# Performance work log

Hardware: AMD Instinct MI355X
Metric: run time of the kernel (lower is better)

## Reference

```python
import jax, jax.numpy as jnp
import numpy as np

FEATS = 1024
HEAD = 16
MLP_HIDDEN = 4096
B, N = 8, 1024
EPS = 1e-5


def _layernorm(x, g, b):
    mu = jnp.mean(x, axis=-1, keepdims=True)
    var = jnp.var(x, axis=-1, keepdims=True)
    return (x - mu) * jax.lax.rsqrt(var + EPS) * g + b


def setup_inputs() -> dict:
    key = jax.random.key(0)
    ks = jax.random.split(key, 12)
    s_attn = 1.0 / np.sqrt(FEATS)
    s_mlp1 = 1.0 / np.sqrt(FEATS)
    s_mlp2 = 1.0 / np.sqrt(MLP_HIDDEN)
    return {
        "x": jax.random.normal(ks[0], (B, N, FEATS), dtype=jnp.float32),
        "ln1_g": jnp.ones((FEATS,), jnp.float32),
        "ln1_b": jnp.zeros((FEATS,), jnp.float32),
        "wq": jax.random.normal(ks[1], (FEATS, FEATS), jnp.float32) * s_attn,
        "bq": jnp.zeros((FEATS,), jnp.float32),
        "wk": jax.random.normal(ks[2], (FEATS, FEATS), jnp.float32) * s_attn,
        "bk": jnp.zeros((FEATS,), jnp.float32),
        "wv": jax.random.normal(ks[3], (FEATS, FEATS), jnp.float32) * s_attn,
        "bv": jnp.zeros((FEATS,), jnp.float32),
        "wo": jax.random.normal(ks[4], (FEATS, FEATS), jnp.float32) * s_attn,
        "bo": jnp.zeros((FEATS,), jnp.float32),
        "ln2_g": jnp.ones((FEATS,), jnp.float32),
        "ln2_b": jnp.zeros((FEATS,), jnp.float32),
        "w1": jax.random.normal(ks[5], (FEATS, MLP_HIDDEN), jnp.float32) * s_mlp1,
        "b1": jnp.zeros((MLP_HIDDEN,), jnp.float32),
        "w2": jax.random.normal(ks[6], (MLP_HIDDEN, FEATS), jnp.float32) * s_mlp2,
        "b2": jnp.zeros((FEATS,), jnp.float32),
    }


def reference(x, ln1_g, ln1_b, wq, bq, wk, bk, wv, bv, wo, bo,
              ln2_g, ln2_b, w1, b1, w2, b2):
    b, n, f = x.shape
    d = f // HEAD
    sqrt_d = jnp.asarray(f, x.dtype) ** 0.5  # NOTE: scale by sqrt(feats), as in source

    h = _layernorm(x, ln1_g, ln1_b)
    # [b, n, f] -> [b, head, n, d]
    q = (h @ wq + bq).reshape(b, n, HEAD, d).transpose(0, 2, 1, 3)
    k = (h @ wk + bk).reshape(b, n, HEAD, d).transpose(0, 2, 1, 3)
    v = (h @ wv + bv).reshape(b, n, HEAD, d).transpose(0, 2, 1, 3)

    score = jnp.einsum('bhif,bhjf->bhij', q, k) / sqrt_d
    p = jax.nn.softmax(score, axis=-1)
    attn = jnp.einsum('bhij,bhjf->bihf', p, v).reshape(b, n, f)
    o = attn @ wo + bo
    out = o + x

    h2 = _layernorm(out, ln2_g, ln2_b)
    m = jax.nn.gelu(h2 @ w1 + b1, approximate=False)
    m = jax.nn.gelu(m @ w2 + b2, approximate=False)
    return m + out
```

## Files before the change

### kernel.cpp

```cpp
#include <hip/hip_runtime.h>
#include <cstdint>

typedef __bf16 bf16;
typedef __attribute__((ext_vector_type(8))) __bf16 bf16x8;
typedef __attribute__((ext_vector_type(4))) __bf16 bf16x4;
typedef __attribute__((ext_vector_type(4))) float f32x4;
typedef __attribute__((ext_vector_type(8))) unsigned short u16x8;

#define AS1C(p) ((const __attribute__((address_space(1))) void*)(p))
#define AS3(p)  ((__attribute__((address_space(3))) void*)(p))

__device__ __forceinline__ float gelu_exact(float v) {
    return 0.5f * v * (1.0f + erff(v * 0.7071067811865476f));
}

__global__ __launch_bounds__(256, 1) void wtrans_kernel(
    const float* __restrict__ w, bf16* __restrict__ wt, int K, int N)
{
    __shared__ float tile[64][65];
    const int k0 = blockIdx.y * 64, n0 = blockIdx.x * 64;
    const int tid = threadIdx.x;
    {
        const int kl = tid >> 2, nc = (tid & 3) * 16;
        #pragma unroll
        for (int i = 0; i < 4; ++i) {
            const float4 v = *(const float4*)&w[(size_t)(k0 + kl) * N + n0 + nc + i * 4];
            tile[kl][nc + i * 4 + 0] = v.x;
            tile[kl][nc + i * 4 + 1] = v.y;
            tile[kl][nc + i * 4 + 2] = v.z;
            tile[kl][nc + i * 4 + 3] = v.w;
        }
    }
    __syncthreads();
    {
        const int nl = tid >> 2, kc = (tid & 3) * 16;
        #pragma unroll
        for (int i = 0; i < 4; ++i) {
            bf16x4 o4;
            o4[0] = (bf16)tile[kc + i * 4 + 0][nl];
            o4[1] = (bf16)tile[kc + i * 4 + 1][nl];
            o4[2] = (bf16)tile[kc + i * 4 + 2][nl];
            o4[3] = (bf16)tile[kc + i * 4 + 3][nl];
            *(bf16x4*)&wt[(size_t)(n0 + nl) * K + k0 + kc + i * 4] = o4;
        }
    }
}

__global__ void bias3_kernel(const float* __restrict__ a, const float* __restrict__ b,
                             const float* __restrict__ c, float* __restrict__ o)
{
    const int i = blockIdx.x * 256 + threadIdx.x;
    o[i] = (i < 1024) ? a[i] : (i < 2048 ? b[i - 1024] : c[i - 2048]);
}

__global__ __launch_bounds__(256, 1) void ln_kernel(
    const float* __restrict__ x, const float* __restrict__ gw,
    const float* __restrict__ bw, bf16* __restrict__ out)
{
    const int row = blockIdx.x, tid = threadIdx.x;
    const float4 v = *(const float4*)&x[(size_t)row * 1024 + tid * 4];
    float s = v.x + v.y + v.z + v.w;
    float q = v.x * v.x + v.y * v.y + v.z * v.z + v.w * v.w;
    #pragma unroll
    for (int off = 32; off > 0; off >>= 1) {
        s += __shfl_xor(s, off);
        q += __shfl_xor(q, off);
    }
    __shared__ float red[8];
    if ((tid & 63) == 0) { red[tid >> 6] = s; red[4 + (tid >> 6)] = q; }
    __syncthreads();
    s = red[0] + red[1] + red[2] + red[3];
    q = red[4] + red[5] + red[6] + red[7];
    const float mu = s * (1.f / 1024.f);
    const float rs = rsqrtf(q * (1.f / 1024.f) - mu * mu + 1e-5f);
    const float4 gg = *(const float4*)&gw[tid * 4];
    const float4 bb = *(const float4*)&bw[tid * 4];
    bf16x4 o4;
    o4[0] = (bf16)((v.x - mu) * rs * gg.x + bb.x);
    o4[1] = (bf16)((v.y - mu) * rs * gg.y + bb.y);
    o4[2] = (bf16)((v.z - mu) * rs * gg.z + bb.z);
    o4[3] = (bf16)((v.w - mu) * rs * gg.w + bb.w);
    *(bf16x4*)&out[(size_t)row * 1024 + tid * 4] = o4;
}

template<int EPI>
__global__ __launch_bounds__(512, 2) void gemm_v7_kernel(
    const bf16* __restrict__ A, const bf16* __restrict__ BT,
    const float* __restrict__ bias, const float* __restrict__ res,
    void* __restrict__ out, int M, int N, int K)
{
    constexpr int ABYTES = 256 * 128;
    constexpr int BUFB = 384 * 128;
    extern __shared__ char lds[];

    const int tid = threadIdx.x;
    const int lane = tid & 63, wid = tid >> 6;
    const int wr = wid >> 1, wc = wid & 1;
    const int j = lane & 15, g = lane >> 4;
    const int skc = ((tid & 7) ^ ((tid >> 4) & 7)) << 3;

    const int nbn = N >> 7;
    const int nwg = (M >> 8) * nbn;
    const int bid = blockIdx.x;
    const int wg = (bid & 7) * (nwg >> 3) + (bid >> 3);
    const int bm = (wg / nbn) << 8;
    const int bn = (wg % nbn) << 7;

    auto stage = [&](int k0, char* obuf) {
        #pragma unroll
        for (int ga = 0; ga < 4; ++ga) {
            const bf16* src = A + (size_t)(bm + ga * 64 + (tid >> 3)) * K + k0 + skc;
            __builtin_amdgcn_global_load_lds(AS1C(src), AS3(obuf + ga * 8192 + tid * 16), 16, 0, 0);
        }
        #pragma unroll
        for (int gb = 0; gb < 2; ++gb) {
            const bf16* src = BT + (size_t)(bn + gb * 64 + (tid >> 3)) * K + k0 + skc;
            __builtin_amdgcn_global_load_lds(AS1C(src), AS3(obuf + ABYTES + gb * 8192 + tid * 16), 16, 0, 0);
        }
    };

    f32x4 acc[4][4] = {};
    const int NT = K >> 6;

    stage(0, lds);
    stage(64, lds + BUFB);
    asm volatile("s_waitcnt vmcnt(6)" ::: "memory");
    __builtin_amdgcn_s_barrier();

    int cur = 0;
    for (int t = 0; t < NT; ++t) {
        char* buf = lds + cur * BUFB;
        const int nxt2 = (cur >= 1) ? cur - 1 : 2;

        bf16x8 af[4][2], bfr[2][2];
        #pragma unroll
        for (int mf = 0; mf < 4; ++mf)
            #pragma unroll
            for (int ks = 0; ks < 2; ++ks) {
                const int R = wr * 64 + mf * 16 + j;
                uint32_t lb = (uint32_t)(R * 128 + ks * 64 + g * 16);
                lb ^= (lb >> 4) & 0x70u;
                af[mf][ks] = *(const bf16x8*)(buf + lb);
            }
        #pragma unroll
        for (int nf = 0; nf < 2; ++nf)
            #pragma unroll
            for (int ks = 0; ks < 2; ++ks) {
                const int R = wc * 64 + nf * 16 + j;
                uint32_t lb = (uint32_t)(R * 128 + ks * 64 + g * 16);
                lb ^= (lb >> 4) & 0x70u;
                bfr[nf][ks] = *(const bf16x8*)(buf + ABYTES + lb);
            }
        if (t + 2 < NT) stage((t + 2) << 6, lds + nxt2 * BUFB);
        __builtin_amdgcn_s_barrier();
        asm volatile("s_waitcnt lgkmcnt(0)" ::: "memory");
        __builtin_amdgcn_sched_barrier(0);
        __builtin_amdgcn_s_setprio(1);
        #pragma unroll
        for (int mf = 0; mf < 4; ++mf)
            #pragma unroll
            for (int nf = 0; nf < 2; ++nf)
                #pragma unroll
                for (int ks = 0; ks < 2; ++ks)
                    acc[mf][nf] = __builtin_amdgcn_mfma_f32_16x16x32_bf16(
                        af[mf][ks], bfr[nf][ks], acc[mf][nf], 0, 0, 0);
        __builtin_amdgcn_s_setprio(0);
        __builtin_amdgcn_s_barrier();

        bf16x8 bfr2[2][2];
        #pragma unroll
        for (int nf = 0; nf < 2; ++nf)
            #pragma unroll
            for (int ks = 0; ks < 2; ++ks) {
                const int R = wc * 64 + (2 + nf) * 16 + j;
                uint32_t lb = (uint32_t)(R * 128 + ks * 64 + g * 16);
                lb ^= (lb >> 4) & 0x70u;
                bfr2[nf][ks] = *(const bf16x8*)(buf + ABYTES + lb);
            }
        __builtin_amdgcn_s_barrier();
        asm volatile("s_waitcnt lgkmcnt(0)" ::: "memory");
        __builtin_amdgcn_sched_barrier(0);
        __builtin_amdgcn_s_setprio(1);
        #pragma unroll
        for (int mf = 0; mf < 4; ++mf)
            #pragma unroll
            for (int nf = 0; nf < 2; ++nf)
                #pragma unroll
                for (int ks = 0; ks < 2; ++ks)
                    acc[mf][2 + nf] = __builtin_amdgcn_mfma_f32_16x16x32_bf16(
                        af[mf][ks], bfr2[nf][ks], acc[mf][2 + nf], 0, 0, 0);
        __builtin_amdgcn_s_setprio(0);
        if (t + 2 < NT) asm volatile("s_waitcnt vmcnt(6)" ::: "memory");
        else            asm volatile("s_waitcnt vmcnt(0)" ::: "memory");
        __builtin_amdgcn_s_barrier();

        cur = (cur == 2) ? 0 : cur + 1;
    }

    const int row0 = bm + wr * 64;
    const int col0 = bn + wc * 64;
    #pragma unroll
    for (int nf = 0; nf < 4; ++nf) {
        const int col = col0 + nf * 16 + j;
        const float bs = bias[col];
        #pragma unroll
        for (int mf = 0; mf < 4; ++mf) {
            #pragma unroll
            for (int r = 0; r < 4; ++r) {
                const int row = row0 + mf * 16 + g * 4 + r;
                float v = acc[mf][nf][r] + bs;
                if constexpr (EPI == 2 || EPI == 3) v = gelu_exact(v);
                if constexpr (EPI == 1 || EPI == 3) {
                    v += res[(size_t)row * N + col];
                    ((float*)out)[(size_t)row * N + col] = v;
                } else {
                    ((bf16*)out)[(size_t)row * N + col] = (bf16)v;
                }
            }
        }
    }
}

__device__ __forceinline__ void attn_iter(
    int c, const bf16* __restrict__ Kp, const bf16* __restrict__ Vp,
    uint32_t (&vTu)[4][64][36],
    bf16x8 (&kf)[4][2], bf16x8 (&kfn)[4][2],
    const bf16x8& qf0, const bf16x8& qf1,
    f32x4 (&o)[4], float& mrun, float& lsum,
    int kp, int d0, int jperm, int g, int j)
{
    const f32x4 zero = {0.f, 0.f, 0.f, 0.f};
    const bool pfv = (c + 2 < 16);
    const bool pfk = (c + 1 < 16);

    u16x8 r0, r1;
    if (pfv) {
        const size_t vb = (size_t)((c + 2) * 64 + kp) * 3072 + d0;
        r0 = *(const u16x8*)&Vp[vb];
        r1 = *(const u16x8*)&Vp[vb + 3072];
    }

    f32x4 s[4];
    #pragma unroll
    for (int t = 0; t < 4; ++t) {
        s[t] = __builtin_amdgcn_mfma_f32_16x16x32_bf16(kf[t][0], qf0, zero, 0, 0, 0);
        s[t] = __builtin_amdgcn_mfma_f32_16x16x32_bf16(kf[t][1], qf1, s[t], 0, 0, 0);
    }

    if (pfk) {
        #pragma unroll
        for (int t = 0; t < 4; ++t) {
            const int key = (c + 1) * 64 + (t >> 1) * 32 + jperm + (t & 1) * 4;
            kfn[t][0] = *(const bf16x8*)&Kp[(size_t)key * 3072 + g * 8];
            kfn[t][1] = *(const bf16x8*)&Kp[(size_t)key * 3072 + 32 + g * 8];
        }
    }

    float cur = fmaxf(fmaxf(s[0][0], s[0][1]), fmaxf(s[0][2], s[0][3]));
    #pragma unroll
    for (int t = 1; t < 4; ++t)
        cur = fmaxf(cur, fmaxf(fmaxf(s[t][0], s[t][1]), fmaxf(s[t][2], s[t][3])));
    cur = fmaxf(cur, __shfl_xor(cur, 16));
    cur = fmaxf(cur, __shfl_xor(cur, 32));

    if (!__all(cur - mrun <= 8.0f)) {
        const float mnew = fmaxf(mrun, cur);
        const float alpha = __expf(mrun - mnew);
        float al[4];
        #pragma unroll
        for (int r = 0; r < 4; ++r) al[r] = __shfl(alpha, g * 4 + r);
        #pragma unroll
        for (int dt = 0; dt < 4; ++dt)
            #pragma unroll
            for (int r = 0; r < 4; ++r) o[dt][r] *= al[r];
        lsum *= alpha;
        mrun = mnew;
    }
    float ps = 0.f;
    #pragma unroll
    for (int t = 0; t < 4; ++t)
        #pragma unroll
        for (int r = 0; r < 4; ++r) {
            const float p = __expf(s[t][r] - mrun);
            s[t][r] = p;
            ps += p;
        }
    lsum += ps;

    bf16x8 pa0, pa1;
    #pragma unroll
    for (int r = 0; r < 4; ++r) {
        pa0[r]     = (bf16)s[0][r];
        pa0[4 + r] = (bf16)s[1][r];
        pa1[r]     = (bf16)s[2][r];
        pa1[4 + r] = (bf16)s[3][r];
    }

    if (pfv) {
        const int wb = (c + 2) & 3;
        #pragma unroll
        for (int i = 0; i < 8; ++i)
            vTu[wb][d0 + i][kp >> 1] = (uint32_t)r0[i] | ((uint32_t)r1[i] << 16);
    }

    const int rb = c & 3;
    #pragma unroll
    for (int dt = 0; dt < 4; ++dt) {
        const bf16* vrow = (const bf16*)&vTu[rb][dt * 16 + j][0];
        const bf16x8 vb0 = *(const bf16x8*)(vrow + g * 8);
        const bf16x8 vb1 = *(const bf16x8*)(vrow + 32 + g * 8);
        o[dt] = __builtin_amdgcn_mfma_f32_16x16x32_bf16(pa0, vb0, o[dt], 0, 0, 0);
        o[dt] = __builtin_amdgcn_mfma_f32_16x16x32_bf16(pa1, vb1, o[dt], 0, 0, 0);
    }
}

__global__ __launch_bounds__(256, 1) void attn_kernel(
    const bf16* __restrict__ qkv, bf16* __restrict__ attn, int bh_base)
{
    const int tid = threadIdx.x;
    const int lane = tid & 63, wid = tid >> 6;
    const int j = lane & 15, g = lane >> 4;

    const int lin = blockIdx.x + blockIdx.y * 16;
    const int virt = (lin & 7) * 128 + (lin >> 3);
    const int bh = bh_base + (virt >> 4), qt = virt & 15;
    const int b = bh >> 4, h = bh & 15;
    const int q0 = qt * 64 + wid * 16;

    const bf16* Qp = qkv + (size_t)b * 1024 * 3072 + h * 64;
    const bf16* Kp = Qp + 1024;
    const bf16* Vp = Qp + 2048;

    __shared__ __attribute__((aligned(16))) uint32_t vTu[4][64][36];

    const int kp = (tid & 31) * 2;
    const int d0 = (tid >> 5) * 8;
    #pragma unroll
    for (int pb = 0; pb < 2; ++pb) {
        const u16x8 r0 = *(const u16x8*)&Vp[(size_t)(pb * 64 + kp) * 3072 + d0];
        const u16x8 r1 = *(const u16x8*)&Vp[(size_t)(pb * 64 + kp + 1) * 3072 + d0];
        #pragma unroll
        for (int i = 0; i < 8; ++i)
            vTu[pb][d0 + i][kp >> 1] = (uint32_t)r0[i] | ((uint32_t)r1[i] << 16);
    }

    bf16x8 qf0 = *(const bf16x8*)&Qp[(size_t)(q0 + j) * 3072 + g * 8];
    bf16x8 qf1 = *(const bf16x8*)&Qp[(size_t)(q0 + j) * 3072 + 32 + g * 8];
    #pragma unroll
    for (int e = 0; e < 8; ++e) {
        qf0[e] = (bf16)((float)qf0[e] * 0.03125f);
        qf1[e] = (bf16)((float)qf1[e] * 0.03125f);
    }

    const int jperm = (j >> 2) * 8 + (j & 3);

    f32x4 o[4] = {};
    float mrun = -1e30f, lsum = 0.f;

    bf16x8 kfA[4][2], kfB[4][2];
    #pragma unroll
    for (int t = 0; t < 4; ++t) {
        const int key = (t >> 1) * 32 + jperm + (t & 1) * 4;
        kfA[t][0] = *(const bf16x8*)&Kp[(size_t)key * 3072 + g * 8];
        kfA[t][1] = *(const bf16x8*)&Kp[(size_t)key * 3072 + 32 + g * 8];
    }

    asm volatile("s_waitcnt lgkmcnt(0)" ::: "memory");
    __builtin_amdgcn_s_barrier();

    for (int cc = 0; cc < 16; cc += 2) {
        attn_iter(cc,     Kp, Vp, vTu, kfA, kfB, qf0, qf1, o, mrun, lsum, kp, d0, jperm, g, j);
        attn_iter(cc + 1, Kp, Vp, vTu, kfB, kfA, qf0, qf1, o, mrun, lsum, kp, d0, jperm, g, j);
        asm volatile("s_waitcnt lgkmcnt(0)" ::: "memory");
        __builtin_amdgcn_sched_barrier(0);
        __builtin_amdgcn_s_barrier();
    }

    lsum += __shfl_xor(lsum, 16);
    lsum += __shfl_xor(lsum, 32);
    float inv[4];
    #pragma unroll
    for (int r = 0; r < 4; ++r) inv[r] = 1.0f / __shfl(lsum, g * 4 + r);
    #pragma unroll
    for (int dt = 0; dt < 4; ++dt)
        #pragma unroll
        for (int r = 0; r < 4; ++r)
            attn[(size_t)(b * 1024 + q0 + g * 4 + r) * 1024 + h * 64 + dt * 16 + j] =
                (bf16)(o[dt][r] * inv[r]);
}

extern "C" void kernel_launch(void* const* d_in, const int* in_sizes, int n_in,
                              void* d_out, int out_size, void* d_ws, size_t ws_size,
                              hipStream_t stream)
{
    const float* x    = (const float*)d_in[0];
    const float* ln1g = (const float*)d_in[1];
    const float* ln1b = (const float*)d_in[2];
    const float* wq   = (const float*)d_in[3];
    const float* bq   = (const float*)d_in[4];
    const float* wk   = (const float*)d_in[5];
    const float* bk   = (const float*)d_in[6];
    const float* wv   = (const float*)d_in[7];
    const float* bv   = (const float*)d_in[8];
    const float* wo   = (const float*)d_in[9];
    const float* bo   = (const float*)d_in[10];
    const float* ln2g = (const float*)d_in[11];
    const float* ln2b = (const float*)d_in[12];
    const float* w1   = (const float*)d_in[13];
    const float* b1   = (const float*)d_in[14];
    const float* w2   = (const float*)d_in[15];
    const float* b2   = (const float*)d_in[16];

    char* ws = (char*)d_ws;
    bf16* wqkvT = (bf16*)ws;  ws += (size_t)3072 * 1024 * 2;
    bf16* woT   = (bf16*)ws;  ws += (size_t)1024 * 1024 * 2;
    bf16* w1T   = (bf16*)ws;  ws += (size_t)4096 * 1024 * 2;
    bf16* w2T   = (bf16*)ws;  ws += (size_t)1024 * 4096 * 2;
    float* bqkv = (float*)ws; ws += (size_t)3072 * 4;
    bf16* h     = (bf16*)ws;  ws += (size_t)8192 * 1024 * 2;
    bf16* qkv   = (bf16*)ws;  ws += (size_t)8192 * 3072 * 2;
    bf16* attn  = (bf16*)ws;  ws += (size_t)8192 * 1024 * 2;
    float* outf = (float*)ws; ws += (size_t)8192 * 1024 * 4;
    bf16* m1    = (bf16*)ws;  ws += (size_t)8192 * 4096 * 2;

    (void)hipFuncSetAttribute((const void*)gemm_v7_kernel<0>,
                              hipFuncAttributeMaxDynamicSharedMemorySize, 147456);
    (void)hipFuncSetAttribute((const void*)gemm_v7_kernel<1>,
                              hipFuncAttributeMaxDynamicSharedMemorySize, 147456);
    (void)hipFuncSetAttribute((const void*)gemm_v7_kernel<2>,
                              hipFuncAttributeMaxDynamicSharedMemorySize, 147456);
    (void)hipFuncSetAttribute((const void*)gemm_v7_kernel<3>,
                              hipFuncAttributeMaxDynamicSharedMemorySize, 147456);

    wtrans_kernel<<<dim3(16, 16), 256, 0, stream>>>(wq, wqkvT,                   1024, 1024);
    wtrans_kernel<<<dim3(16, 16), 256, 0, stream>>>(wk, wqkvT + 1024 * 1024,     1024, 1024);
    wtrans_kernel<<<dim3(16, 16), 256, 0, stream>>>(wv, wqkvT + 2 * 1024 * 1024, 1024, 1024);
    wtrans_kernel<<<dim3(16, 16), 256, 0, stream>>>(wo, woT, 1024, 1024);
    wtrans_kernel<<<dim3(64, 16), 256, 0, stream>>>(w1, w1T, 1024, 4096);
    wtrans_kernel<<<dim3(16, 64), 256, 0, stream>>>(w2, w2T, 4096, 1024);
    bias3_kernel<<<12, 256, 0, stream>>>(bq, bk, bv, bqkv);

    ln_kernel<<<8192, 256, 0, stream>>>(x, ln1g, ln1b, h);
    gemm_v7_kernel<0><<<768, 512, 147456, stream>>>(h, wqkvT, bqkv, nullptr, qkv, 8192, 3072, 1024);
    attn_kernel<<<dim3(16, 64), 256, 0, stream>>>(qkv, attn, 0);
    attn_kernel<<<dim3(16, 64), 256, 0, stream>>>(qkv, attn, 64);
    gemm_v7_kernel<1><<<256, 512, 147456, stream>>>(attn, woT, bo, x, outf, 8192, 1024, 1024);
    ln_kernel<<<8192, 256, 0, stream>>>(outf, ln2g, ln2b, h);
    gemm_v7_kernel<2><<<1024, 512, 147456, stream>>>(h, w1T, b1, nullptr, m1, 8192, 4096, 1024);
    gemm_v7_kernel<3><<<256, 512, 147456, stream>>>(m1, w2T, b2, outf, (float*)d_out, 8192, 1024, 4096);
}
```

Baseline: 511.9 us.

## Restructure GEMM to K=32 steps with 4-stage ring and register double-buffered fragments

The bf16 GEMM kernel now steps through K in chunks of 32 instead of 64. It uses a four-deep LDS ring (three stages prefetched) and a new XOR swizzle, and cuts dynamic LDS per block from 144 KB to 96 KB. Fragments for the next tile are read from LDS into a second register set while MFMAs run on the current one, so LDS reads overlap compute and there are fewer barriers per MFMA batch. In exchange it needs more loop iterations and barriers over K and a finer vmcnt/lgkmcnt bookkeeping, which could add overhead or hide latency less well.

New measurement: 545.4 us. +6.5%, slower.

```diff
diff --git a/kernel.cpp b/kernel.cpp
--- a/kernel.cpp
+++ b/kernel.cpp
@@ -84,117 +84,100 @@
 }
 
 template<int EPI>
-__global__ __launch_bounds__(512, 2) void gemm_v7_kernel(
+__global__ __launch_bounds__(512, 2) void gemm_v8_kernel(
     const bf16* __restrict__ A, const bf16* __restrict__ BT,
     const float* __restrict__ bias, const float* __restrict__ res,
     void* __restrict__ out, int M, int N, int K)
 {
-    constexpr int ABYTES = 256 * 128;
-    constexpr int BUFB = 384 * 128;
+    constexpr int ABYTES = 256 * 64;
+    constexpr int BUFB = 384 * 64;
     extern __shared__ char lds[];
 
     const int tid = threadIdx.x;
     const int lane = tid & 63, wid = tid >> 6;
     const int wr = wid >> 1, wc = wid & 1;
     const int j = lane & 15, g = lane >> 4;
-    const int skc = ((tid & 7) ^ ((tid >> 4) & 7)) << 3;
+    const int srow = tid >> 2;
+    const int skc = (((tid & 3) ^ ((tid >> 2) & 3)) << 3);
 
     const int nbn = N >> 7;
     const int nwg = (M >> 8) * nbn;
-    const int bid = blockIdx.x;
-    const int wg = (bid & 7) * (nwg >> 3) + (bid >> 3);
+    const int wg = (blockIdx.x & 7) * (nwg >> 3) + (blockIdx.x >> 3);
     const int bm = (wg / nbn) << 8;
     const int bn = (wg % nbn) << 7;
 
-    auto stage = [&](int k0, char* obuf) {
-        #pragma unroll
-        for (int ga = 0; ga < 4; ++ga) {
-            const bf16* src = A + (size_t)(bm + ga * 64 + (tid >> 3)) * K + k0 + skc;
-            __builtin_amdgcn_global_load_lds(AS1C(src), AS3(obuf + ga * 8192 + tid * 16), 16, 0, 0);
-        }
-        #pragma unroll
-        for (int gb = 0; gb < 2; ++gb) {
-            const bf16* src = BT + (size_t)(bn + gb * 64 + (tid >> 3)) * K + k0 + skc;
-            __builtin_amdgcn_global_load_lds(AS1C(src), AS3(obuf + ABYTES + gb * 8192 + tid * 16), 16, 0, 0);
-        }
+    const int NT = K >> 5;
+
+    auto stage = [&](int t) {
+        char* obuf = lds + (t & 3) * BUFB;
+        const int k0 = t << 5;
+        const bf16* sA0 = A + (size_t)(bm + srow) * K + k0 + skc;
+        __builtin_amdgcn_global_load_lds(AS1C(sA0), AS3(obuf + tid * 16), 16, 0, 0);
+        const bf16* sA1 = A + (size_t)(bm + 128 + srow) * K + k0 + skc;
+        __builtin_amdgcn_global_load_lds(AS1C(sA1), AS3(obuf + 8192 + tid * 16), 16, 0, 0);
+        const bf16* sB = BT + (size_t)(bn + srow) * K + k0 + skc;
+        __builtin_amdgcn_global_load_lds(AS1C(sB), AS3(obuf + ABYTES + tid * 16), 16, 0, 0);
     };
+    auto rdA = [&](char* buf, int mf) {
+        const int R = wr * 64 + mf * 16 + j;
+        uint32_t lb = (uint32_t)(R * 64 + g * 16);
+        lb ^= ((lb >> 6) & 3u) << 4;
+        return *(const bf16x8*)(buf + lb);
+    };
+    auto rdB = [&](char* buf, int nf) {
+        const int R = wc * 64 + nf * 16 + j;
+        uint32_t lb = (uint32_t)(R * 64 + g * 16);
+        lb ^= ((lb >> 6) & 3u) << 4;
+        return *(const bf16x8*)(buf + ABYTES + lb);
+    };
 
     f32x4 acc[4][4] = {};
-    const int NT = K >> 6;
-
-    stage(0, lds);
-    stage(64, lds + BUFB);
+
+    stage(0); stage(1); stage(2);
     asm volatile("s_waitcnt vmcnt(6)" ::: "memory");
     __builtin_amdgcn_s_barrier();
-
-    int cur = 0;
-    for (int t = 0; t < NT; ++t) {
-        char* buf = lds + cur * BUFB;
-        const int nxt2 = (cur >= 1) ? cur - 1 : 2;
-
-        bf16x8 af[4][2], bfr[2][2];
+    __builtin_amdgcn_sched_barrier(0);
+    bf16x8 afX[4], bfX[4], afY[4], bfY[4];
+    #pragma unroll
+    for (int mf = 0; mf < 4; ++mf) afX[mf] = rdA(lds, mf);
+    #pragma unroll
+    for (int nf = 0; nf < 4; ++nf) bfX[nf] = rdB(lds, nf);
+
+    auto body = [&](int t, bf16x8 (&afc)[4], bf16x8 (&bfc)[4],
+                    bf16x8 (&afn)[4], bf16x8 (&bfn)[4]) {
+        if (t + 3 < NT) stage(t + 3);
+        if (t + 1 < NT) {
+            if (t + 3 < NT)      asm volatile("s_waitcnt vmcnt(6)" ::: "memory");
+            else if (t + 2 < NT) asm volatile("s_waitcnt vmcnt(3)" ::: "memory");
+            else                 asm volatile("s_waitcnt vmcnt(0)" ::: "memory");
+        }
+        __builtin_amdgcn_s_barrier();
+        __builtin_amdgcn_sched_barrier(0);
+        if (t + 1 < NT) {
+            char* nbuf = lds + ((t + 1) & 3) * BUFB;
+            #pragma unroll
+            for (int mf = 0; mf < 4; ++mf) afn[mf] = rdA(nbuf, mf);
+            #pragma unroll
+            for (int nf = 0; nf < 4; ++nf) bfn[nf] = rdB(nbuf, nf);
+            asm volatile("s_waitcnt lgkmcnt(8)" ::: "memory");
+        } else {
+            asm volatile("s_waitcnt lgkmcnt(0)" ::: "memory");
+        }
+        __builtin_amdgcn_sched_barrier(0);
+        __builtin_amdgcn_s_setprio(1);
         #pragma unroll
         for (int mf = 0; mf < 4; ++mf)
             #pragma unroll
-            for (int ks = 0; ks < 2; ++ks) {
-                const int R = wr * 64 + mf * 16 + j;
-                uint32_t lb = (uint32_t)(R * 128 + ks * 64 + g * 16);
-                lb ^= (lb >> 4) & 0x70u;
-                af[mf][ks] = *(const bf16x8*)(buf + lb);
-            }
-        #pragma unroll
-        for (int nf = 0; nf < 2; ++nf)
-            #pragma unroll
-            for (int ks = 0; ks < 2; ++ks) {
-                const int R = wc * 64 + nf * 16 + j;
-                uint32_t lb = (uint32_t)(R * 128 + ks * 64 + g * 16);
-                lb ^= (lb >> 4) & 0x70u;
-                bfr[nf][ks] = *(const bf16x8*)(buf + ABYTES + lb);
-            }
-        if (t + 2 < NT) stage((t + 2) << 6, lds + nxt2 * BUFB);
-        __builtin_amdgcn_s_barrier();
-        asm volatile("s_waitcnt lgkmcnt(0)" ::: "memory");
-        __builtin_amdgcn_sched_barrier(0);
-        __builtin_amdgcn_s_setprio(1);
-        #pragma unroll
-        for (int mf = 0; mf < 4; ++mf)
-            #pragma unroll
-            for (int nf = 0; nf < 2; ++nf)
-                #pragma unroll
-                for (int ks = 0; ks < 2; ++ks)
-                    acc[mf][nf] = __builtin_amdgcn_mfma_f32_16x16x32_bf16(
-                        af[mf][ks], bfr[nf][ks], acc[mf][nf], 0, 0, 0);
+            for (int nf = 0; nf < 4; ++nf)
+                acc[mf][nf] = __builtin_amdgcn_mfma_f32_16x16x32_bf16(
+                    afc[mf], bfc[nf], acc[mf][nf], 0, 0, 0);
         __builtin_amdgcn_s_setprio(0);
         __builtin_amdgcn_s_barrier();
-
-        bf16x8 bfr2[2][2];
-        #pragma unroll
-        for (int nf = 0; nf < 2; ++nf)
-            #pragma unroll
-            for (int ks = 0; ks < 2; ++ks) {
-                const int R = wc * 64 + (2 + nf) * 16 + j;
-                uint32_t lb = (uint32_t)(R * 128 + ks * 64 + g * 16);
-                lb ^= (lb >> 4) & 0x70u;
-                bfr2[nf][ks] = *(const bf16x8*)(buf + ABYTES + lb);
-            }
-        __builtin_amdgcn_s_barrier();
-        asm volatile("s_waitcnt lgkmcnt(0)" ::: "memory");
-        __builtin_amdgcn_sched_barrier(0);
-        __builtin_amdgcn_s_setprio(1);
-        #pragma unroll
-        for (int mf = 0; mf < 4; ++mf)
-            #pragma unroll
-            for (int nf = 0; nf < 2; ++nf)
-                #pragma unroll
-                for (int ks = 0; ks < 2; ++ks)
-                    acc[mf][2 + nf] = __builtin_amdgcn_mfma_f32_16x16x32_bf16(
-                        af[mf][ks], bfr2[nf][ks], acc[mf][2 + nf], 0, 0, 0);
-        __builtin_amdgcn_s_setprio(0);
-        if (t + 2 < NT) asm volatile("s_waitcnt vmcnt(6)" ::: "memory");
-        else            asm volatile("s_waitcnt vmcnt(0)" ::: "memory");
-        __builtin_amdgcn_s_barrier();
-
-        cur = (cur == 2) ? 0 : cur + 1;
+    };
+
+    for (int t = 0; t < NT; t += 2) {
+        body(t,     afX, bfX, afY, bfY);
+        body(t + 1, afY, bfY, afX, bfX);
     }
 
     const int row0 = bm + wr * 64;
@@ -423,14 +406,14 @@
     float* outf = (float*)ws; ws += (size_t)8192 * 1024 * 4;
     bf16* m1    = (bf16*)ws;  ws += (size_t)8192 * 4096 * 2;
 
-    (void)hipFuncSetAttribute((const void*)gemm_v7_kernel<0>,
-                              hipFuncAttributeMaxDynamicSharedMemorySize, 147456);
-    (void)hipFuncSetAttribute((const void*)gemm_v7_kernel<1>,
-                              hipFuncAttributeMaxDynamicSharedMemorySize, 147456);
-    (void)hipFuncSetAttribute((const void*)gemm_v7_kernel<2>,
-                              hipFuncAttributeMaxDynamicSharedMemorySize, 147456);
-    (void)hipFuncSetAttribute((const void*)gemm_v7_kernel<3>,
-                              hipFuncAttributeMaxDynamicSharedMemorySize, 147456);
+    (void)hipFuncSetAttribute((const void*)gemm_v8_kernel<0>,
+                              hipFuncAttributeMaxDynamicSharedMemorySize, 98304);
+    (void)hipFuncSetAttribute((const void*)gemm_v8_kernel<1>,
+                              hipFuncAttributeMaxDynamicSharedMemorySize, 98304);
+    (void)hipFuncSetAttribute((const void*)gemm_v8_kernel<2>,
+                              hipFuncAttributeMaxDynamicSharedMemorySize, 98304);
+    (void)hipFuncSetAttribute((const void*)gemm_v8_kernel<3>,
+                              hipFuncAttributeMaxDynamicSharedMemorySize, 98304);
 
     wtrans_kernel<<<dim3(16, 16), 256, 0, stream>>>(wq, wqkvT,                   1024, 1024);
     wtrans_kernel<<<dim3(16, 16), 256, 0, stream>>>(wk, wqkvT + 1024 * 1024,     1024, 1024);
@@ -441,11 +424,11 @@
     bias3_kernel<<<12, 256, 0, stream>>>(bq, bk, bv, bqkv);
 
     ln_kernel<<<8192, 256, 0, stream>>>(x, ln1g, ln1b, h);
-    gemm_v7_kernel<0><<<768, 512, 147456, stream>>>(h, wqkvT, bqkv, nullptr, qkv, 8192, 3072, 1024);
+    gemm_v8_kernel<0><<<768, 512, 98304, stream>>>(h, wqkvT, bqkv, nullptr, qkv, 8192, 3072, 1024);
     attn_kernel<<<dim3(16, 64), 256, 0, stream>>>(qkv, attn, 0);
     attn_kernel<<<dim3(16, 64), 256, 0, stream>>>(qkv, attn, 64);
-    gemm_v7_kernel<1><<<256, 512, 147456, stream>>>(attn, woT, bo, x, outf, 8192, 1024, 1024);
+    gemm_v8_kernel<1><<<256, 512, 98304, stream>>>(attn, woT, bo, x, outf, 8192, 1024, 1024);
     ln_kernel<<<8192, 256, 0, stream>>>(outf, ln2g, ln2b, h);
-    gemm_v7_kernel<2><<<1024, 512, 147456, stream>>>(h, w1T, b1, nullptr, m1, 8192, 4096, 1024);
-    gemm_v7_kernel<3><<<256, 512, 147456, stream>>>(m1, w2T, b2, outf, (float*)d_out, 8192, 1024, 4096);
-}
+    gemm_v8_kernel<2><<<1024, 512, 98304, stream>>>(h, w1T, b1, nullptr, m1, 8192, 4096, 1024);
+    gemm_v8_kernel<3><<<256, 512, 98304, stream>>>(m1, w2T, b2, outf, (float*)d_out, 8192, 1024, 4096);
+}
```

## Process two query tiles per attention wave to reuse K/V fragments

Applied to the files above, without the earlier changes.

Each attention block now handles 128 query rows instead of 64: every wave keeps two independent 16-row query tiles with separate running max, sum and output accumulators. The K fragments and the transposed V tile in LDS are shared by both tiles, which halves the K/V global loads and LDS transposes per query row. The grid is halved to match. This raises register pressure and leaves fewer blocks per launch (512 per launch), which may leave CUs underused.

After: 449.9 us. 1.14x faster.

```diff
diff --git a/kernel.cpp b/kernel.cpp
--- a/kernel.cpp
+++ b/kernel.cpp
@@ -221,99 +221,6 @@
     }
 }
 
-__device__ __forceinline__ void attn_iter(
-    int c, const bf16* __restrict__ Kp, const bf16* __restrict__ Vp,
-    uint32_t (&vTu)[4][64][36],
-    bf16x8 (&kf)[4][2], bf16x8 (&kfn)[4][2],
-    const bf16x8& qf0, const bf16x8& qf1,
-    f32x4 (&o)[4], float& mrun, float& lsum,
-    int kp, int d0, int jperm, int g, int j)
-{
-    const f32x4 zero = {0.f, 0.f, 0.f, 0.f};
-    const bool pfv = (c + 2 < 16);
-    const bool pfk = (c + 1 < 16);
-
-    u16x8 r0, r1;
-    if (pfv) {
-        const size_t vb = (size_t)((c + 2) * 64 + kp) * 3072 + d0;
-        r0 = *(const u16x8*)&Vp[vb];
-        r1 = *(const u16x8*)&Vp[vb + 3072];
-    }
-
-    f32x4 s[4];
-    #pragma unroll
-    for (int t = 0; t < 4; ++t) {
-        s[t] = __builtin_amdgcn_mfma_f32_16x16x32_bf16(kf[t][0], qf0, zero, 0, 0, 0);
-        s[t] = __builtin_amdgcn_mfma_f32_16x16x32_bf16(kf[t][1], qf1, s[t], 0, 0, 0);
-    }
-
-    if (pfk) {
-        #pragma unroll
-        for (int t = 0; t < 4; ++t) {
-            const int key = (c + 1) * 64 + (t >> 1) * 32 + jperm + (t & 1) * 4;
-            kfn[t][0] = *(const bf16x8*)&Kp[(size_t)key * 3072 + g * 8];
-            kfn[t][1] = *(const bf16x8*)&Kp[(size_t)key * 3072 + 32 + g * 8];
-        }
-    }
-
-    float cur = fmaxf(fmaxf(s[0][0], s[0][1]), fmaxf(s[0][2], s[0][3]));
-    #pragma unroll
-    for (int t = 1; t < 4; ++t)
-        cur = fmaxf(cur, fmaxf(fmaxf(s[t][0], s[t][1]), fmaxf(s[t][2], s[t][3])));
-    cur = fmaxf(cur, __shfl_xor(cur, 16));
-    cur = fmaxf(cur, __shfl_xor(cur, 32));
-
-    if (!__all(cur - mrun <= 8.0f)) {
-        const float mnew = fmaxf(mrun, cur);
-        const float alpha = __expf(mrun - mnew);
-        float al[4];
-        #pragma unroll
-        for (int r = 0; r < 4; ++r) al[r] = __shfl(alpha, g * 4 + r);
-        #pragma unroll
-        for (int dt = 0; dt < 4; ++dt)
-            #pragma unroll
-            for (int r = 0; r < 4; ++r) o[dt][r] *= al[r];
-        lsum *= alpha;
-        mrun = mnew;
-    }
-    float ps = 0.f;
-    #pragma unroll
-    for (int t = 0; t < 4; ++t)
-        #pragma unroll
-        for (int r = 0; r < 4; ++r) {
-            const float p = __expf(s[t][r] - mrun);
-            s[t][r] = p;
-            ps += p;
-        }
-    lsum += ps;
-
-    bf16x8 pa0, pa1;
-    #pragma unroll
-    for (int r = 0; r < 4; ++r) {
-        pa0[r]     = (bf16)s[0][r];
-        pa0[4 + r] = (bf16)s[1][r];
-        pa1[r]     = (bf16)s[2][r];
-        pa1[4 + r] = (bf16)s[3][r];
-    }
-
-    if (pfv) {
-        const int wb = (c + 2) & 3;
-        #pragma unroll
-        for (int i = 0; i < 8; ++i)
-            vTu[wb][d0 + i][kp >> 1] = (uint32_t)r0[i] | ((uint32_t)r1[i] << 16);
-    }
-
-    const int rb = c & 3;
-    #pragma unroll
-    for (int dt = 0; dt < 4; ++dt) {
-        const bf16* vrow = (const bf16*)&vTu[rb][dt * 16 + j][0];
-        const bf16x8 vb0 = *(const bf16x8*)(vrow + g * 8);
-        const bf16x8 vb1 = *(const bf16x8*)(vrow + 32 + g * 8);
-        o[dt] = __builtin_amdgcn_mfma_f32_16x16x32_bf16(pa0, vb0, o[dt], 0, 0, 0);
-        o[dt] = __builtin_amdgcn_mfma_f32_16x16x32_bf16(pa1, vb1, o[dt], 0, 0, 0);
-    }
-}
-
 __global__ __launch_bounds__(256, 1) void attn_kernel(
     const bf16* __restrict__ qkv, bf16* __restrict__ attn, int bh_base)
 {
@@ -321,11 +228,12 @@
     const int lane = tid & 63, wid = tid >> 6;
     const int j = lane & 15, g = lane >> 4;
 
-    const int lin = blockIdx.x + blockIdx.y * 16;
-    const int virt = (lin & 7) * 128 + (lin >> 3);
-    const int bh = bh_base + (virt >> 4), qt = virt & 15;
+    const int lin = blockIdx.x + blockIdx.y * 8;
+    const int virt = (lin & 7) * 64 + (lin >> 3);
+    const int bh = bh_base + (virt >> 3), qp = virt & 7;
     const int b = bh >> 4, h = bh & 15;
-    const int q0 = qt * 64 + wid * 16;
+    const int q0a = qp * 128 + wid * 16;
+    const int q0b = q0a + 64;
 
     const bf16* Qp = qkv + (size_t)b * 1024 * 3072 + h * 64;
     const bf16* Kp = Qp + 1024;
@@ -344,18 +252,23 @@
             vTu[pb][d0 + i][kp >> 1] = (uint32_t)r0[i] | ((uint32_t)r1[i] << 16);
     }
 
-    bf16x8 qf0 = *(const bf16x8*)&Qp[(size_t)(q0 + j) * 3072 + g * 8];
-    bf16x8 qf1 = *(const bf16x8*)&Qp[(size_t)(q0 + j) * 3072 + 32 + g * 8];
+    bf16x8 qa0 = *(const bf16x8*)&Qp[(size_t)(q0a + j) * 3072 + g * 8];
+    bf16x8 qa1 = *(const bf16x8*)&Qp[(size_t)(q0a + j) * 3072 + 32 + g * 8];
+    bf16x8 qb0 = *(const bf16x8*)&Qp[(size_t)(q0b + j) * 3072 + g * 8];
+    bf16x8 qb1 = *(const bf16x8*)&Qp[(size_t)(q0b + j) * 3072 + 32 + g * 8];
     #pragma unroll
     for (int e = 0; e < 8; ++e) {
-        qf0[e] = (bf16)((float)qf0[e] * 0.03125f);
-        qf1[e] = (bf16)((float)qf1[e] * 0.03125f);
+        qa0[e] = (bf16)((float)qa0[e] * 0.03125f);
+        qa1[e] = (bf16)((float)qa1[e] * 0.03125f);
+        qb0[e] = (bf16)((float)qb0[e] * 0.03125f);
+        qb1[e] = (bf16)((float)qb1[e] * 0.03125f);
     }
 
     const int jperm = (j >> 2) * 8 + (j & 3);
 
-    f32x4 o[4] = {};
-    float mrun = -1e30f, lsum = 0.f;
+    f32x4 oa[4] = {}, ob[4] = {};
+    float mra = -1e30f, lsa = 0.f;
+    float mrb = -1e30f, lsb = 0.f;
 
     bf16x8 kfA[4][2], kfB[4][2];
     #pragma unroll
@@ -368,25 +281,131 @@
     asm volatile("s_waitcnt lgkmcnt(0)" ::: "memory");
     __builtin_amdgcn_s_barrier();
 
+    auto softmax = [&](f32x4 (&s)[4], float& mrun, float& lsum, f32x4 (&o)[4]) {
+        float cur = fmaxf(fmaxf(s[0][0], s[0][1]), fmaxf(s[0][2], s[0][3]));
+        #pragma unroll
+        for (int t = 1; t < 4; ++t)
+            cur = fmaxf(cur, fmaxf(fmaxf(s[t][0], s[t][1]), fmaxf(s[t][2], s[t][3])));
+        cur = fmaxf(cur, __shfl_xor(cur, 16));
+        cur = fmaxf(cur, __shfl_xor(cur, 32));
+        if (!__all(cur - mrun <= 8.0f)) {
+            const float mnew = fmaxf(mrun, cur);
+            const float alpha = __expf(mrun - mnew);
+            float al[4];
+            #pragma unroll
+            for (int r = 0; r < 4; ++r) al[r] = __shfl(alpha, g * 4 + r);
+            #pragma unroll
+            for (int dt = 0; dt < 4; ++dt)
+                #pragma unroll
+                for (int r = 0; r < 4; ++r) o[dt][r] *= al[r];
+            lsum *= alpha;
+            mrun = mnew;
+        }
+        float ps = 0.f;
+        #pragma unroll
+        for (int t = 0; t < 4; ++t)
+            #pragma unroll
+            for (int r = 0; r < 4; ++r) {
+                const float p = __expf(s[t][r] - mrun);
+                s[t][r] = p;
+                ps += p;
+            }
+        lsum += ps;
+    };
+
+    auto iter = [&](int c, bf16x8 (&kf)[4][2], bf16x8 (&kfn)[4][2]) {
+        const f32x4 zero = {0.f, 0.f, 0.f, 0.f};
+        const bool pfv = (c + 2 < 16);
+        const bool pfk = (c + 1 < 16);
+
+        u16x8 r0, r1;
+        if (pfv) {
+            const size_t vb = (size_t)((c + 2) * 64 + kp) * 3072 + d0;
+            r0 = *(const u16x8*)&Vp[vb];
+            r1 = *(const u16x8*)&Vp[vb + 3072];
+        }
+
+        f32x4 sa[4], sb[4];
+        #pragma unroll
+        for (int t = 0; t < 4; ++t) {
+            sa[t] = __builtin_amdgcn_mfma_f32_16x16x32_bf16(kf[t][0], qa0, zero, 0, 0, 0);
+            sb[t] = __builtin_amdgcn_mfma_f32_16x16x32_bf16(kf[t][0], qb0, zero, 0, 0, 0);
+            sa[t] = __builtin_amdgcn_mfma_f32_16x16x32_bf16(kf[t][1], qa1, sa[t], 0, 0, 0);
+            sb[t] = __builtin_amdgcn_mfma_f32_16x16x32_bf16(kf[t][1], qb1, sb[t], 0, 0, 0);
+        }
+
+        if (pfk) {
+            #pragma unroll
+            for (int t = 0; t < 4; ++t) {
+                const int key = (c + 1) * 64 + (t >> 1) * 32 + jperm + (t & 1) * 4;
+                kfn[t][0] = *(const bf16x8*)&Kp[(size_t)key * 3072 + g * 8];
+                kfn[t][1] = *(const bf16x8*)&Kp[(size_t)key * 3072 + 32 + g * 8];
+            }
+        }
+
+        softmax(sa, mra, lsa, oa);
+        softmax(sb, mrb, lsb, ob);
+
+        bf16x8 paa0, paa1, pab0, pab1;
+        #pragma unroll
+        for (int r = 0; r < 4; ++r) {
+            paa0[r]     = (bf16)sa[0][r];
+            paa0[4 + r] = (bf16)sa[1][r];
+            paa1[r]     = (bf16)sa[2][r];
+            paa1[4 + r] = (bf16)sa[3][r];
+            pab0[r]     = (bf16)sb[0][r];
+            pab0[4 + r] = (bf16)sb[1][r];
+            pab1[r]     = (bf16)sb[2][r];
+            pab1[4 + r] = (bf16)sb[3][r];
+        }
+
+        if (pfv) {
+            const int wb = (c + 2) & 3;
+            #pragma unroll
+            for (int i = 0; i < 8; ++i)
+                vTu[wb][d0 + i][kp >> 1] = (uint32_t)r0[i] | ((uint32_t)r1[i] << 16);
+        }
+
+        const int rb = c & 3;
+        #pragma unroll
+        for (int dt = 0; dt < 4; ++dt) {
+            const bf16* vrow = (const bf16*)&vTu[rb][dt * 16 + j][0];
+            const bf16x8 vb0 = *(const bf16x8*)(vrow + g * 8);
+            const bf16x8 vb1 = *(const bf16x8*)(vrow + 32 + g * 8);
+            oa[dt] = __builtin_amdgcn_mfma_f32_16x16x32_bf16(paa0, vb0, oa[dt], 0, 0, 0);
+            ob[dt] = __builtin_amdgcn_mfma_f32_16x16x32_bf16(pab0, vb0, ob[dt], 0, 0, 0);
+            oa[dt] = __builtin_amdgcn_mfma_f32_16x16x32_bf16(paa1, vb1, oa[dt], 0, 0, 0);
+            ob[dt] = __builtin_amdgcn_mfma_f32_16x16x32_bf16(pab1, vb1, ob[dt], 0, 0, 0);
+        }
+    };
+
     for (int cc = 0; cc < 16; cc += 2) {
-        attn_iter(cc,     Kp, Vp, vTu, kfA, kfB, qf0, qf1, o, mrun, lsum, kp, d0, jperm, g, j);
-        attn_iter(cc + 1, Kp, Vp, vTu, kfB, kfA, qf0, qf1, o, mrun, lsum, kp, d0, jperm, g, j);
+        iter(cc,     kfA, kfB);
+        iter(cc + 1, kfB, kfA);
         asm volatile("s_waitcnt lgkmcnt(0)" ::: "memory");
         __builtin_amdgcn_sched_barrier(0);
         __builtin_amdgcn_s_barrier();
     }
 
-    lsum += __shfl_xor(lsum, 16);
-    lsum += __shfl_xor(lsum, 32);
-    float inv[4];
-    #pragma unroll
-    for (int r = 0; r < 4; ++r) inv[r] = 1.0f / __shfl(lsum, g * 4 + r);
+    lsa += __shfl_xor(lsa, 16);
+    lsa += __shfl_xor(lsa, 32);
+    lsb += __shfl_xor(lsb, 16);
+    lsb += __shfl_xor(lsb, 32);
+    float inva[4], invb[4];
+    #pragma unroll
+    for (int r = 0; r < 4; ++r) {
+        inva[r] = 1.0f / __shfl(lsa, g * 4 + r);
+        invb[r] = 1.0f / __shfl(lsb, g * 4 + r);
+    }
     #pragma unroll
     for (int dt = 0; dt < 4; ++dt)
         #pragma unroll
-        for (int r = 0; r < 4; ++r)
-            attn[(size_t)(b * 1024 + q0 + g * 4 + r) * 1024 + h * 64 + dt * 16 + j] =
-                (bf16)(o[dt][r] * inv[r]);
+        for (int r = 0; r < 4; ++r) {
+            attn[(size_t)(b * 1024 + q0a + g * 4 + r) * 1024 + h * 64 + dt * 16 + j] =
+                (bf16)(oa[dt][r] * inva[r]);
+            attn[(size_t)(b * 1024 + q0b + g * 4 + r) * 1024 + h * 64 + dt * 16 + j] =
+                (bf16)(ob[dt][r] * invb[r]);
+        }
 }
 
 extern "C" void kernel_launch(void* const* d_in, const int* in_sizes, int n_in,
@@ -442,8 +461,8 @@
 
     ln_kernel<<<8192, 256, 0, stream>>>(x, ln1g, ln1b, h);
     gemm_v7_kernel<0><<<768, 512, 147456, stream>>>(h, wqkvT, bqkv, nullptr, qkv, 8192, 3072, 1024);
-    attn_kernel<<<dim3(16, 64), 256, 0, stream>>>(qkv, attn, 0);
-    attn_kernel<<<dim3(16, 64), 256, 0, stream>>>(qkv, attn, 64);
+    attn_kernel<<<dim3(8, 64), 256, 0, stream>>>(qkv, attn, 0);
+    attn_kernel<<<dim3(8, 64), 256, 0, stream>>>(qkv, attn, 64);
     gemm_v7_kernel<1><<<256, 512, 147456, stream>>>(attn, woT, bo, x, outf, 8192, 1024, 1024);
     ln_kernel<<<8192, 256, 0, stream>>>(outf, ln2g, ln2b, h);
     gemm_v7_kernel<2><<<1024, 512, 147456, stream>>>(h, w1T, b1, nullptr, m1, 8192, 4096, 1024);
```
